# Kernel tuning notes

Measured on AMD Instinct MI355X. Metric: run time of the kernel, lower is better.

Reference implementation:

```python
import jax, jax.numpy as jnp
import numpy as np

DIM = 256
HEADS = 8
GROUPS = 4
HIDDEN = int(DIM * 4.0)
GW = DIM // GROUPS          # group width = 64
HEAD_DIM = DIM // HEADS     # 32
SCALE = HEAD_DIM ** (-0.5)
LN_EPS = 1e-6
BN_EPS = 1e-3               # keras BatchNormalization default epsilon
L2_EPS = 1e-12              # tf.nn.l2_normalize default


def _l2norm(t):
    ss = jnp.sum(t * t, axis=-1, keepdims=True)
    return t * jax.lax.rsqrt(jnp.maximum(ss, L2_EPS))


def setup_inputs() -> dict:
    key = jax.random.key(0)
    ks = jax.random.split(key, 12)
    B, H, W = 16, 56, 56
    x = jax.random.normal(ks[0], (B, H, W, DIM), jnp.float32)
    # depthwise 3x3 kernels for groups 1..GROUPS-1 (group 0's conv is unused in the
    # original code: y0 is a plain slice). Combined depthwise kernel over the last
    # (GROUPS-1)*GW channels, keras HWIO layout with in_ch_per_group = 1.
    dw_kernel = jax.random.normal(ks[1], (3, 3, 1, (GROUPS - 1) * GW), jnp.float32) * 0.05
    dw_bias = jnp.zeros(((GROUPS - 1) * GW,), jnp.float32)
    ln_gamma = jnp.ones((DIM,), jnp.float32)
    ln_beta = jnp.zeros((DIM,), jnp.float32)
    qkv_w = jax.random.normal(ks[2], (DIM, 3 * DIM), jnp.float32) * 0.02  # qkv_bias=False
    proj_w = jax.random.normal(ks[3], (DIM, DIM), jnp.float32) * 0.02
    proj_b = jnp.zeros((DIM,), jnp.float32)
    bn_gamma = jnp.ones((DIM,), jnp.float32)
    bn_beta = jnp.zeros((DIM,), jnp.float32)
    bn_mean = jax.random.normal(ks[4], (DIM,), jnp.float32) * 0.1
    bn_var = jax.random.uniform(ks[5], (DIM,), jnp.float32, 0.5, 1.5)
    fc1_w = jax.random.normal(ks[6], (DIM, HIDDEN), jnp.float32) * 0.02
    fc1_b = jnp.zeros((HIDDEN,), jnp.float32)
    fc2_w = jax.random.normal(ks[7], (HIDDEN, DIM), jnp.float32) * 0.02
    fc2_b = jnp.zeros((DIM,), jnp.float32)
    return dict(x=x, dw_kernel=dw_kernel, dw_bias=dw_bias, ln_gamma=ln_gamma,
                ln_beta=ln_beta, qkv_w=qkv_w, proj_w=proj_w, proj_b=proj_b,
                bn_gamma=bn_gamma, bn_beta=bn_beta, bn_mean=bn_mean, bn_var=bn_var,
                fc1_w=fc1_w, fc1_b=fc1_b, fc2_w=fc2_w, fc2_b=fc2_b)


def _gdta_forward(x, dw_kernel, dw_bias, ln_gamma, ln_beta, qkv_w, proj_w, proj_b,
                  bn_gamma, bn_beta, bn_mean, bn_var, fc1_w, fc1_b, fc2_w, fc2_b):
    B, H, W, C = x.shape
    N = H * W
    # ---- GOTA_block_part1: grouped depthwise convs with cumulative residual ----
    # y0 = x[..., :GW]; for i>=1: K_i = dwconv_i(x_i); y1=K1, y_i = K_i + y_{i-1}
    # => y_i (i>=1) is the cumulative sum of K_1..K_i along the group axis.
    xc = x[..., GW:]  # [B,H,W,(G-1)*GW]
    K = jax.lax.conv_general_dilated(
        xc, dw_kernel, window_strides=(1, 1), padding='SAME',
        dimension_numbers=('NHWC', 'HWIO', 'NHWC'),
        feature_group_count=(GROUPS - 1) * GW) + dw_bias
    Kg = K.reshape(B, H, W, GROUPS - 1, GW)
    Yg = jnp.cumsum(Kg, axis=3).reshape(B, H, W, (GROUPS - 1) * GW)
    dwconv = jnp.concatenate([x[..., :GW], Yg], axis=-1)  # [B,H,W,C]
    # ---- LayerNorm (last axis) ----
    mu = jnp.mean(dwconv, axis=-1, keepdims=True)
    var = jnp.mean(jnp.square(dwconv - mu), axis=-1, keepdims=True)
    norm1 = (dwconv - mu) * jax.lax.rsqrt(var + LN_EPS) * ln_gamma + ln_beta
    t = norm1.reshape(B, N, C)
    # ---- channel (cross-covariance) attention ----
    qkv = (t @ qkv_w).reshape(B, N, 3, HEADS, HEAD_DIM)
    qkv = jnp.transpose(qkv, (2, 0, 3, 1, 4))  # [3,B,h,N,d]
    q, k, v = qkv[0], qkv[1], qkv[2]
    q = _l2norm(q) * SCALE
    k = _l2norm(k)
    attn = jnp.einsum('bhnd,bhne->bhde', q, k)       # [B,h,d,d]
    attn = jax.nn.softmax(attn, axis=-1)
    out = jnp.einsum('bhnd,bhde->bhne', v, attn)     # [B,h,N,d]
    out = jnp.transpose(out, (0, 2, 1, 3)).reshape(B, N, C)
    out = out @ proj_w + proj_b
    attn_img = out.reshape(B, H, W, C)
    # ---- merge + BatchNorm (inference) + MLP + residual ----
    merged = attn_img + dwconv
    merged = (merged - bn_mean) * jax.lax.rsqrt(bn_var + BN_EPS) * bn_gamma + bn_beta
    h1 = jax.nn.gelu(merged @ fc1_w + fc1_b, approximate=False)
    mlp = h1 @ fc2_w + fc2_b
    return x + mlp


def reference(x, dw_kernel, dw_bias, ln_gamma, ln_beta, qkv_w, proj_w, proj_b,
              bn_gamma, bn_beta, bn_mean, bn_var, fc1_w, fc1_b, fc2_w, fc2_b):
    return _gdta_forward(x, dw_kernel, dw_bias, ln_gamma, ln_beta, qkv_w, proj_w,
                         proj_b, bn_gamma, bn_beta, bn_mean, bn_var,
                         fc1_w, fc1_b, fc2_w, fc2_b)
```

## Files before the change

### kernel.cpp

```cpp
#include <hip/hip_runtime.h>
#include <cstdint>

typedef unsigned short u16;
typedef __attribute__((ext_vector_type(8))) _Float16 f16x8;
typedef __attribute__((ext_vector_type(8))) unsigned short u16x8;
typedef __attribute__((ext_vector_type(4))) float f32x4;

#define SPLITN 7

__device__ __forceinline__ float b2f(u16 u) {
  union { unsigned int i; float f; } v; v.i = ((unsigned int)u) << 16; return v.f;
}
__device__ __forceinline__ u16 f2b(float f) {
  union { float f; unsigned int i; } v; v.f = f;
  unsigned int x = v.i;
  return (u16)((x + 0x7fffu + ((x >> 16) & 1u)) >> 16);
}
__device__ __forceinline__ u16 f2h(float f) {
  union { _Float16 h; u16 u; } v; v.h = (_Float16)f; return v.u;
}
__device__ __forceinline__ float h2f(u16 u) {
  union { u16 u; _Float16 h; } v; v.u = u; return (float)v.h;
}
__device__ __forceinline__ float ld(const void* p, long i, int f) {
  return f ? ((const float*)p)[i] : b2f(((const u16*)p)[i]);
}
template<int F>
__device__ __forceinline__ float4 ld4(const void* p, long i) {
  if (F) return *(const float4*)((const float*)p + i);
  const ushort4 u = *(const ushort4*)((const u16*)p + i);
  return make_float4(b2f(u.x), b2f(u.y), b2f(u.z), b2f(u.w));
}

__global__ __launch_bounds__(256) void detect_kernel(const u16* __restrict__ x,
                                                     int* __restrict__ flag) {
  __shared__ int sbad;
  if (threadIdx.x == 0) sbad = 0;
  __syncthreads();
  int b = 0;
  #pragma unroll
  for (int rr = 0; rr < 2; ++rr) {
    const int i = rr * 256 + threadIdx.x;
    const float v = fabsf(b2f(x[2 * i]));
    if (!(v < 100.f) || v < 1e-6f) ++b;
  }
  atomicAdd(&sbad, b);
  __syncthreads();
  if (threadIdx.x == 0) *flag = (sbad > 16) ? 1 : 0;
}

__global__ void transpose_cvt_kernel(const void* __restrict__ w0, u16* __restrict__ o0,
                                     const void* __restrict__ w1, u16* __restrict__ o1,
                                     const void* __restrict__ w2, u16* __restrict__ o2,
                                     const int* __restrict__ flagp) {
  const int f = *flagp;
  int bb = blockIdx.x;
  const void* in; u16* out; int R, C;
  if (bb < 768)       { in = w0; out = o0; R = 256;  C = 768;  }
  else if (bb < 1792) { in = w1; out = o1; R = 256;  C = 1024; bb -= 768; }
  else                { in = w2; out = o2; R = 1024; C = 256;  bb -= 1792; }
  const int o = bb * 256 + threadIdx.x;
  if (o < R * C) {
    const int i = o / R, j = o % R;
    out[o] = f2h(ld(in, (long)j * C + i, f));
  }
}

template<int F>
__device__ __forceinline__ void dwconv_body(
    const void* __restrict__ x, const void* __restrict__ dwk, const void* __restrict__ dwb,
    const void* __restrict__ lng, const void* __restrict__ lnb,
    u16* __restrict__ dwc, u16* __restrict__ norm1, int tok, int lane)
{
  const int b = tok / 3136, rem = tok % 3136;
  const int hh = rem / 56, ww = rem % 56;
  const long row0 = (long)tok * 256;
  const int c0 = lane * 4;
  const float4 xv = ld4<F>(x, row0 + c0);
  float sx = 0.f, sy = 0.f, sz = 0.f, sw = 0.f;
  if (lane >= 16) {
    const int j0 = c0 - 64;
    const float4 bb = ld4<F>(dwb, j0);
    sx = bb.x; sy = bb.y; sz = bb.z; sw = bb.w;
    #pragma unroll
    for (int dh = -1; dh <= 1; ++dh) {
      const int h2 = hh + dh;
      if (h2 < 0 || h2 >= 56) continue;
      #pragma unroll
      for (int dw2 = -1; dw2 <= 1; ++dw2) {
        const int w2 = ww + dw2;
        if (w2 < 0 || w2 >= 56) continue;
        const long nb = ((long)b * 3136 + h2 * 56 + w2) * 256;
        const float4 xt = ld4<F>(x, nb + c0);
        const float4 wt = ld4<F>(dwk, (long)((dh + 1) * 3 + (dw2 + 1)) * 192 + j0);
        sx += xt.x * wt.x; sy += xt.y * wt.y; sz += xt.z * wt.z; sw += xt.w * wt.w;
      }
    }
  }
  const float t1x = __shfl(sx, lane - 16), t1y = __shfl(sy, lane - 16),
              t1z = __shfl(sz, lane - 16), t1w = __shfl(sw, lane - 16);
  const float t2x = __shfl(sx, lane - 32), t2y = __shfl(sy, lane - 32),
              t2z = __shfl(sz, lane - 32), t2w = __shfl(sw, lane - 32);
  if (lane >= 32) { sx += t1x; sy += t1y; sz += t1z; sw += t1w; }
  if (lane >= 48) { sx += t2x; sy += t2y; sz += t2z; sw += t2w; }
  float vx, vy, vz, vw;
  if (lane < 16) { vx = xv.x; vy = xv.y; vz = xv.z; vw = xv.w; }
  else           { vx = sx;   vy = sy;   vz = sz;   vw = sw;   }
  float sum = vx + vy + vz + vw;
  float sq = vx * vx + vy * vy + vz * vz + vw * vw;
  #pragma unroll
  for (int m = 32; m; m >>= 1) { sum += __shfl_xor(sum, m); sq += __shfl_xor(sq, m); }
  const float mu = sum * (1.0f / 256.0f);
  const float var = sq * (1.0f / 256.0f) - mu * mu;
  const float rstd = rsqrtf(fmaxf(var, 0.f) + 1e-6f);
  const float4 g = ld4<F>(lng, c0);
  const float4 be = ld4<F>(lnb, c0);
  ushort4 dv, nv;
  dv.x = f2h(vx); dv.y = f2h(vy); dv.z = f2h(vz); dv.w = f2h(vw);
  nv.x = f2h((vx - mu) * rstd * g.x + be.x);
  nv.y = f2h((vy - mu) * rstd * g.y + be.y);
  nv.z = f2h((vz - mu) * rstd * g.z + be.z);
  nv.w = f2h((vw - mu) * rstd * g.w + be.w);
  *(ushort4*)(dwc + row0 + c0) = dv;
  *(ushort4*)(norm1 + row0 + c0) = nv;
}

__global__ __launch_bounds__(256) void dwconv_ln_kernel(
    const void* __restrict__ x, const void* __restrict__ dwk, const void* __restrict__ dwb,
    const void* __restrict__ lng, const void* __restrict__ lnb,
    u16* __restrict__ dwc, u16* __restrict__ norm1, const int* __restrict__ flagp)
{
  const int wave = threadIdx.x >> 6, lane = threadIdx.x & 63;
  const int tok = blockIdx.x * 4 + wave;
  if (*flagp) dwconv_body<1>(x, dwk, dwb, lng, lnb, dwc, norm1, tok, lane);
  else        dwconv_body<0>(x, dwk, dwb, lng, lnb, dwc, norm1, tok, lane);
}

template<int BM, int WR, int WC, int EPI, int KT>
__global__ __launch_bounds__(256) void gemm_kernel(
    const u16* __restrict__ A, const u16* __restrict__ Bt, void* C,
    int lda, int ldb, int ldc,
    long aZ, long bZ, long cZ, long zoff,
    const void* __restrict__ bias, const void* aux,
    const void* __restrict__ bng, const void* __restrict__ bnb,
    const void* __restrict__ bnm, const void* __restrict__ bnv,
    const int* __restrict__ flagp)
{
  static_assert(BM == 64 || BM == 128, "");
  constexpr int BN = 128;
  constexpr int WM = BM / WR, WN = BN / WC;
  constexpr int MI = WM / 16, NI = WN / 16;
  __shared__ __align__(16) u16 As[BM * 32];
  __shared__ __align__(16) u16 Bs[BN * 32];
  const int f = (EPI == 0 || EPI == 5) ? 0 : *flagp;
  const int tid = threadIdx.x;
  const int wave = tid >> 6, lane = tid & 63;
  const int wr = wave / WC, wc = wave % WC;
  const int quad = lane >> 4, l16 = lane & 15;
  const int tileM = blockIdx.y * BM, tileN = blockIdx.x * BN;
  const u16* Ab = A + (long)blockIdx.z * aZ + (long)tileM * lda;
  const u16* Bb = Bt + (long)blockIdx.z * bZ + (long)tileN * ldb;
  const int sr = lane >> 2;
  const int sc = (lane & 3) * 8;
  f32x4 acc[MI][NI];
  #pragma unroll
  for (int mi = 0; mi < MI; ++mi)
    #pragma unroll
    for (int ni = 0; ni < NI; ++ni)
      acc[mi][ni] = (f32x4){0.f, 0.f, 0.f, 0.f};

  for (int k0 = 0; k0 < KT; k0 += 32) {
    #pragma unroll
    for (int j = 0; j < BM / 64; ++j) {
      const int chunk = wave * (BM / 64) + j;
      const u16* g = Ab + (long)(chunk * 16 + sr) * lda + k0 + sc;
      __builtin_amdgcn_global_load_lds(
          (const __attribute__((address_space(1))) void*)g,
          (__attribute__((address_space(3))) void*)(As + chunk * 512), 16, 0, 0);
    }
    #pragma unroll
    for (int j = 0; j < 2; ++j) {
      const int chunk = wave * 2 + j;
      const u16* g = Bb + (long)(chunk * 16 + sr) * ldb + k0 + sc;
      __builtin_amdgcn_global_load_lds(
          (const __attribute__((address_space(1))) void*)g,
          (__attribute__((address_space(3))) void*)(Bs + chunk * 512), 16, 0, 0);
    }
    __syncthreads();
    f16x8 af[MI], bfr[NI];
    #pragma unroll
    for (int mi = 0; mi < MI; ++mi)
      af[mi] = *(const f16x8*)&As[(wr * WM + mi * 16 + l16) * 32 + quad * 8];
    #pragma unroll
    for (int ni = 0; ni < NI; ++ni)
      bfr[ni] = *(const f16x8*)&Bs[(wc * WN + ni * 16 + l16) * 32 + quad * 8];
    #pragma unroll
    for (int mi = 0; mi < MI; ++mi)
      #pragma unroll
      for (int ni = 0; ni < NI; ++ni)
        acc[mi][ni] = __builtin_amdgcn_mfma_f32_16x16x32_f16(af[mi], bfr[ni], acc[mi][ni], 0, 0, 0);
    __syncthreads();
  }

  const long zC = (long)blockIdx.z * cZ + ((EPI == 5) ? 0 : zoff);
  #pragma unroll
  for (int mi = 0; mi < MI; ++mi) {
    #pragma unroll
    for (int ni = 0; ni < NI; ++ni) {
      const int col = tileN + wc * WN + ni * 16 + l16;
      #pragma unroll
      for (int r = 0; r < 4; ++r) {
        const int row = tileM + wr * WM + mi * 16 + quad * 4 + r;
        const long ci = zC + (long)row * ldc + col;
        float v = acc[mi][ni][r];
        if (EPI == 0) {
          ((u16*)C)[ci] = f2h(v);
        } else if (EPI == 2) {
          v += ld(bias, col, f);
          v += h2f(((const u16*)aux)[ci]);
          v = (v - ld(bnm, col, f)) * rsqrtf(ld(bnv, col, f) + 1e-3f) * ld(bng, col, f) + ld(bnb, col, f);
          ((u16*)C)[ci] = f2h(v);
        } else if (EPI == 3) {
          v += ld(bias, col, f);
          v = 0.5f * v * (1.0f + erff(v * 0.7071067811865475f));
          ((u16*)C)[ci] = f2h(v);
        } else if (EPI == 4) {
          v += ld(bias, col, f);
          v += ld(aux, ci, f);
          if (f) ((float*)C)[ci] = v; else ((u16*)C)[ci] = f2b(v);
        } else {
          if (col < 512) ((u16*)C)[(long)row * 512 + col] = f2h(v);
          else ((u16*)aux)[zoff + (long)row * 256 + (col - 512)] = f2h(v);
        }
      }
    }
  }
}

__global__ __launch_bounds__(256) void attn_accum_kernel(
    const u16* __restrict__ qk, float* __restrict__ A_part, int pair0)
{
  const int pl = blockIdx.x;
  const int split = blockIdx.y;
  const int bl = pl >> 3, h = pl & 7;
  const int tid = threadIdx.x;
  const int wave = tid >> 6, lane = tid & 63;
  const int quad = lane >> 4, l16 = lane & 15;
  const int dq = wave >> 1, eq = wave & 1;
  __shared__ __align__(16) u16 lqT[32 * 72];
  __shared__ __align__(16) u16 lkT[32 * 72];
  const long rowbase = (long)bl * 3136 * 512;
  const int n0 = split * 448;
  f32x4 acc = (f32x4){0.f, 0.f, 0.f, 0.f};
  const int seg = tid & 7;

  for (int ch = 0; ch < 7; ++ch) {
    const int nb = n0 + ch * 64;
    #pragma unroll
    for (int rr = 0; rr < 2; ++rr) {
      const int a = rr * 256 + tid;
      const int nl = a >> 3;
      const int co = (seg < 4) ? h * 32 + seg * 8 : 256 + h * 32 + (seg - 4) * 8;
      const u16x8 v8 = *(const u16x8*)(qk + rowbase + (long)(nb + nl) * 512 + co);
      float vf[8], p = 0.f;
      #pragma unroll
      for (int i = 0; i < 8; ++i) { vf[i] = h2f(v8[i]); p += vf[i] * vf[i]; }
      float p1 = p + __shfl_xor(p, 1);
      float p2 = p1 + __shfl_xor(p1, 2);
      const float other = __shfl_xor(p2, 4);
      const float ssq = (seg < 4) ? p2 : other;
      const float ssk = (seg < 4) ? other : p2;
      const float s = 0.17677669529663687f * rsqrtf(fmaxf(ssq, 1e-12f)) *
                      rsqrtf(fmaxf(ssk, 1e-12f));
      if (seg < 4) {
        const int db = seg * 8;
        #pragma unroll
        for (int i = 0; i < 8; ++i) {
          const int d = db + i;
          lqT[d * 72 + (nl ^ (d & 24))] = f2h(vf[i] * s);
        }
      } else {
        const int eb = (seg - 4) * 8;
        #pragma unroll
        for (int i = 0; i < 8; ++i) {
          const int e = eb + i;
          lkT[e * 72 + (nl ^ (e & 24))] = v8[i];
        }
      }
    }
    __syncthreads();
    #pragma unroll
    for (int ks = 0; ks < 2; ++ks) {
      const int tb = ks * 32 + quad * 8;
      const int dA = dq * 16 + l16;
      const int eB = eq * 16 + l16;
      const f16x8 af = *(const f16x8*)&lqT[dA * 72 + (tb ^ (dA & 24))];
      const f16x8 bf = *(const f16x8*)&lkT[eB * 72 + (tb ^ (eB & 24))];
      acc = __builtin_amdgcn_mfma_f32_16x16x32_f16(af, bf, acc, 0, 0, 0);
    }
    __syncthreads();
  }
  float* o = A_part + ((long)(pair0 + pl) * SPLITN + split) * 1024;
  #pragma unroll
  for (int r = 0; r < 4; ++r)
    o[(dq * 16 + quad * 4 + r) * 32 + eq * 16 + l16] = acc[r];
}

__global__ __launch_bounds__(1024) void softmax_kernel(float* A_part) {
  const int pair = blockIdx.x;
  const int t = threadIdx.x;
  float v = 0.f;
  float* base = A_part + (long)pair * SPLITN * 1024 + t;
  #pragma unroll
  for (int s = 0; s < SPLITN; ++s) v += base[s * 1024];
  float mx = v;
  #pragma unroll
  for (int m = 16; m; m >>= 1) mx = fmaxf(mx, __shfl_xor(mx, m, 32));
  const float p = expf(v - mx);
  float sm = p;
  #pragma unroll
  for (int m = 16; m; m >>= 1) sm += __shfl_xor(sm, m, 32);
  base[0] = p / sm;
}

__global__ __launch_bounds__(256) void wb_kernel(
    const float* __restrict__ A_part, const void* __restrict__ proj_w,
    u16* __restrict__ Wbt, const int* __restrict__ flagp)
{
  const int f = *flagp;
  const int b = blockIdx.x;
  const int cs = blockIdx.y;
  const int tid = threadIdx.x;
  const int cg = tid & 31, dg = tid >> 5;
  const int c = cs * 32 + cg;
  __shared__ float Ah[32][32];
  __shared__ float pw[32][33];
  for (int h = 0; h < 8; ++h) {
    const float* Abase = A_part + ((long)(b * 8 + h) * SPLITN) * 1024;
    #pragma unroll
    for (int rr = 0; rr < 4; ++rr) {
      const int ff = rr * 256 + tid;
      Ah[ff >> 5][ff & 31] = Abase[ff];
    }
    #pragma unroll
    for (int rr = 0; rr < 4; ++rr) {
      const int ff = rr * 256 + tid;
      const int e = ff >> 5, ccc = ff & 31;
      pw[e][ccc] = ld(proj_w, (long)(h * 32 + e) * 256 + cs * 32 + ccc, f);
    }
    __syncthreads();
    float acc[4] = {0.f, 0.f, 0.f, 0.f};
    #pragma unroll
    for (int e = 0; e < 32; ++e) {
      const float pv = pw[e][cg];
      #pragma unroll
      for (int dd = 0; dd < 4; ++dd)
        acc[dd] += Ah[dg * 4 + dd][e] * pv;
    }
    #pragma unroll
    for (int dd = 0; dd < 4; ++dd)
      Wbt[((long)b * 256 + c) * 256 + h * 32 + dg * 4 + dd] = f2h(acc[dd]);
    __syncthreads();
  }
}

extern "C" void kernel_launch(void* const* d_in, const int* in_sizes, int n_in,
                              void* d_out, int out_size, void* d_ws, size_t ws_size,
                              hipStream_t stream) {
  const void* x      = d_in[0];
  const void* dwk    = d_in[1];
  const void* dwb    = d_in[2];
  const void* lng    = d_in[3];
  const void* lnb    = d_in[4];
  const void* qkv_w  = d_in[5];
  const void* proj_w = d_in[6];
  const void* proj_b = d_in[7];
  const void* bn_g   = d_in[8];
  const void* bn_b   = d_in[9];
  const void* bn_m   = d_in[10];
  const void* bn_v   = d_in[11];
  const void* fc1_w  = d_in[12];
  const void* fc1_b  = d_in[13];
  const void* fc2_w  = d_in[14];
  const void* fc2_b  = d_in[15];
  char* ws = (char*)d_ws;

  int*   flagp   = (int*)  (ws + 0);
  u16*   wqkvT   = (u16*)  (ws + 256);
  u16*   wfc1T   = (u16*)  (ws + 393472);
  u16*   wfc2T   = (u16*)  (ws + 917760);
  float* A_part  = (float*)(ws + 1442048);
  u16*   Wbt     = (u16*)  (ws + 5112064);
  u16*   vbuf    = (u16*)  (ws + 7209216);
  u16*   dwc     = (u16*)  (ws + 32899328);
  u16*   qk_half = (u16*)  (ws + 58589440);
  u16*   h1c     = (u16*)  (ws + 58589440);
  u16*   norm1   = (u16*)d_out;

  detect_kernel<<<1, 256, 0, stream>>>((const u16*)x, flagp);

  transpose_cvt_kernel<<<2816, 256, 0, stream>>>(qkv_w, wqkvT, fc1_w, wfc1T,
                                                 fc2_w, wfc2T, flagp);

  dwconv_ln_kernel<<<12544, 256, 0, stream>>>(x, dwk, dwb, lng, lnb, dwc, norm1, flagp);

  for (int half = 0; half < 2; ++half) {
    const u16* nh = norm1 + (long)half * 25088 * 256;
    gemm_kernel<128, 2, 2, 5, 256><<<dim3(6, 196, 1), 256, 0, stream>>>(
        nh, wqkvT, qk_half, 256, 256, 512, 0, 0, 0, (long)half * 25088 * 256,
        nullptr, vbuf, nullptr, nullptr, nullptr, nullptr, flagp);
    attn_accum_kernel<<<dim3(64, SPLITN), 256, 0, stream>>>(qk_half, A_part, half * 64);
  }

  softmax_kernel<<<128, 1024, 0, stream>>>(A_part);
  wb_kernel<<<dim3(16, 8), 256, 0, stream>>>(A_part, proj_w, Wbt, flagp);

  gemm_kernel<64, 1, 4, 2, 256><<<dim3(2, 49, 16), 256, 0, stream>>>(
      vbuf, Wbt, dwc, 256, 256, 256,
      (long)3136 * 256, 65536, (long)3136 * 256, 0,
      proj_b, dwc, bn_g, bn_b, bn_m, bn_v, flagp);

  for (int c2 = 0; c2 < 4; ++c2) {
    const long ro = (long)c2 * 12544 * 256;
    gemm_kernel<128, 2, 2, 3, 256><<<dim3(8, 98, 1), 256, 0, stream>>>(
        dwc + ro, wfc1T, h1c, 256, 256, 1024, 0, 0, 0, 0,
        fc1_b, nullptr, nullptr, nullptr, nullptr, nullptr, flagp);
    gemm_kernel<64, 1, 4, 4, 1024><<<dim3(2, 196, 1), 256, 0, stream>>>(
        h1c, wfc2T, d_out, 1024, 1024, 256, 0, 0, 0, ro,
        fc2_b, x, nullptr, nullptr, nullptr, nullptr, flagp);
  }
}
```

Before: 565.8 us.

## Reuse dwconv row loads across four pixels, swizzle GEMM LDS, use tanh GELU

The depthwise conv + LayerNorm kernel now handles four horizontally adjacent tokens per wave and loads a 6-wide row window once per kernel row, so neighbour pixels share the same loads. The launch grid shrinks to match. The GEMM kernel moves to a K-step of 64 with an XOR-swizzled LDS layout to cut bank conflicts and halve the number of barrier rounds. The exact erf GELU in the fc1 epilogue is replaced by the tanh approximation built on __expf, which trades some accuracy for cheaper math.

```diff
diff --git a/kernel.cpp b/kernel.cpp
--- a/kernel.cpp
+++ b/kernel.cpp
@@ -30,6 +30,14 @@
   if (F) return *(const float4*)((const float*)p + i);
   const ushort4 u = *(const ushort4*)((const u16*)p + i);
   return make_float4(b2f(u.x), b2f(u.y), b2f(u.z), b2f(u.w));
+}
+__device__ __forceinline__ void fma4(float4& a, const float4 x, const float4 k) {
+  a.x += x.x * k.x; a.y += x.y * k.y; a.z += x.z * k.z; a.w += x.w * k.w;
+}
+__device__ __forceinline__ float gelu(float v) {
+  const float u = v * (0.7978845608028654f + 0.035677408136300125f * v * v);
+  const float e = __expf(2.0f * u);
+  return 0.5f * v * (1.0f + (1.0f - 2.0f / (e + 1.0f)));
 }
 
 __global__ __launch_bounds__(256) void detect_kernel(const u16* __restrict__ x,
@@ -67,62 +75,78 @@
 }
 
 template<int F>
-__device__ __forceinline__ void dwconv_body(
+__device__ __forceinline__ void dwconv_body4(
     const void* __restrict__ x, const void* __restrict__ dwk, const void* __restrict__ dwb,
     const void* __restrict__ lng, const void* __restrict__ lnb,
-    u16* __restrict__ dwc, u16* __restrict__ norm1, int tok, int lane)
+    u16* __restrict__ dwc, u16* __restrict__ norm1, int tg, int lane)
 {
-  const int b = tok / 3136, rem = tok % 3136;
-  const int hh = rem / 56, ww = rem % 56;
-  const long row0 = (long)tok * 256;
+  const int b = tg / 784, rem = tg % 784;
+  const int hh = rem / 14, wg = (rem % 14) * 4;
   const int c0 = lane * 4;
-  const float4 xv = ld4<F>(x, row0 + c0);
-  float sx = 0.f, sy = 0.f, sz = 0.f, sw = 0.f;
+  const long tok0 = (long)b * 3136 + hh * 56 + wg;
+  float4 acc[4];
+  float4 pv[4];
   if (lane >= 16) {
     const int j0 = c0 - 64;
     const float4 bb = ld4<F>(dwb, j0);
-    sx = bb.x; sy = bb.y; sz = bb.z; sw = bb.w;
+    acc[0] = bb; acc[1] = bb; acc[2] = bb; acc[3] = bb;
     #pragma unroll
     for (int dh = -1; dh <= 1; ++dh) {
       const int h2 = hh + dh;
       if (h2 < 0 || h2 >= 56) continue;
-      #pragma unroll
-      for (int dw2 = -1; dw2 <= 1; ++dw2) {
-        const int w2 = ww + dw2;
-        if (w2 < 0 || w2 >= 56) continue;
-        const long nb = ((long)b * 3136 + h2 * 56 + w2) * 256;
-        const float4 xt = ld4<F>(x, nb + c0);
-        const float4 wt = ld4<F>(dwk, (long)((dh + 1) * 3 + (dw2 + 1)) * 192 + j0);
-        sx += xt.x * wt.x; sy += xt.y * wt.y; sz += xt.z * wt.z; sw += xt.w * wt.w;
+      const long rb = ((long)b * 3136 + h2 * 56) * 256;
+      float4 xr[6];
+      #pragma unroll
+      for (int i = 0; i < 6; ++i) {
+        const int w2 = wg - 1 + i;
+        xr[i] = (w2 >= 0 && w2 < 56) ? ld4<F>(x, rb + (long)w2 * 256 + c0)
+                                     : make_float4(0.f, 0.f, 0.f, 0.f);
       }
-    }
-  }
-  const float t1x = __shfl(sx, lane - 16), t1y = __shfl(sy, lane - 16),
-              t1z = __shfl(sz, lane - 16), t1w = __shfl(sw, lane - 16);
-  const float t2x = __shfl(sx, lane - 32), t2y = __shfl(sy, lane - 32),
-              t2z = __shfl(sz, lane - 32), t2w = __shfl(sw, lane - 32);
-  if (lane >= 32) { sx += t1x; sy += t1y; sz += t1z; sw += t1w; }
-  if (lane >= 48) { sx += t2x; sy += t2y; sz += t2z; sw += t2w; }
-  float vx, vy, vz, vw;
-  if (lane < 16) { vx = xv.x; vy = xv.y; vz = xv.z; vw = xv.w; }
-  else           { vx = sx;   vy = sy;   vz = sz;   vw = sw;   }
-  float sum = vx + vy + vz + vw;
-  float sq = vx * vx + vy * vy + vz * vz + vw * vw;
-  #pragma unroll
-  for (int m = 32; m; m >>= 1) { sum += __shfl_xor(sum, m); sq += __shfl_xor(sq, m); }
-  const float mu = sum * (1.0f / 256.0f);
-  const float var = sq * (1.0f / 256.0f) - mu * mu;
-  const float rstd = rsqrtf(fmaxf(var, 0.f) + 1e-6f);
+      float4 kw[3];
+      #pragma unroll
+      for (int i = 0; i < 3; ++i)
+        kw[i] = ld4<F>(dwk, (long)((dh + 1) * 3 + i) * 192 + j0);
+      #pragma unroll
+      for (int t = 0; t < 4; ++t)
+        #pragma unroll
+        for (int i = 0; i < 3; ++i)
+          fma4(acc[t], xr[t + i], kw[i]);
+    }
+  } else {
+    #pragma unroll
+    for (int t = 0; t < 4; ++t)
+      pv[t] = ld4<F>(x, (tok0 + t) * 256 + c0);
+  }
   const float4 g = ld4<F>(lng, c0);
   const float4 be = ld4<F>(lnb, c0);
-  ushort4 dv, nv;
-  dv.x = f2h(vx); dv.y = f2h(vy); dv.z = f2h(vz); dv.w = f2h(vw);
-  nv.x = f2h((vx - mu) * rstd * g.x + be.x);
-  nv.y = f2h((vy - mu) * rstd * g.y + be.y);
-  nv.z = f2h((vz - mu) * rstd * g.z + be.z);
-  nv.w = f2h((vw - mu) * rstd * g.w + be.w);
-  *(ushort4*)(dwc + row0 + c0) = dv;
-  *(ushort4*)(norm1 + row0 + c0) = nv;
+  #pragma unroll
+  for (int t = 0; t < 4; ++t) {
+    float sx = acc[t].x, sy = acc[t].y, sz = acc[t].z, sw = acc[t].w;
+    const float t1x = __shfl(sx, lane - 16), t1y = __shfl(sy, lane - 16),
+                t1z = __shfl(sz, lane - 16), t1w = __shfl(sw, lane - 16);
+    const float t2x = __shfl(sx, lane - 32), t2y = __shfl(sy, lane - 32),
+                t2z = __shfl(sz, lane - 32), t2w = __shfl(sw, lane - 32);
+    if (lane >= 32) { sx += t1x; sy += t1y; sz += t1z; sw += t1w; }
+    if (lane >= 48) { sx += t2x; sy += t2y; sz += t2z; sw += t2w; }
+    float vx, vy, vz, vw;
+    if (lane < 16) { vx = pv[t].x; vy = pv[t].y; vz = pv[t].z; vw = pv[t].w; }
+    else           { vx = sx;      vy = sy;      vz = sz;      vw = sw;      }
+    float sum = vx + vy + vz + vw;
+    float sq = vx * vx + vy * vy + vz * vz + vw * vw;
+    #pragma unroll
+    for (int m = 32; m; m >>= 1) { sum += __shfl_xor(sum, m); sq += __shfl_xor(sq, m); }
+    const float mu = sum * (1.0f / 256.0f);
+    const float var = sq * (1.0f / 256.0f) - mu * mu;
+    const float rstd = rsqrtf(fmaxf(var, 0.f) + 1e-6f);
+    ushort4 dv, nv;
+    dv.x = f2h(vx); dv.y = f2h(vy); dv.z = f2h(vz); dv.w = f2h(vw);
+    nv.x = f2h((vx - mu) * rstd * g.x + be.x);
+    nv.y = f2h((vy - mu) * rstd * g.y + be.y);
+    nv.z = f2h((vz - mu) * rstd * g.z + be.z);
+    nv.w = f2h((vw - mu) * rstd * g.w + be.w);
+    *(ushort4*)(dwc + (tok0 + t) * 256 + c0) = dv;
+    *(ushort4*)(norm1 + (tok0 + t) * 256 + c0) = nv;
+  }
 }
 
 __global__ __launch_bounds__(256) void dwconv_ln_kernel(
@@ -131,9 +155,9 @@
     u16* __restrict__ dwc, u16* __restrict__ norm1, const int* __restrict__ flagp)
 {
   const int wave = threadIdx.x >> 6, lane = threadIdx.x & 63;
-  const int tok = blockIdx.x * 4 + wave;
-  if (*flagp) dwconv_body<1>(x, dwk, dwb, lng, lnb, dwc, norm1, tok, lane);
-  else        dwconv_body<0>(x, dwk, dwb, lng, lnb, dwc, norm1, tok, lane);
+  const int tg = blockIdx.x * 4 + wave;
+  if (*flagp) dwconv_body4<1>(x, dwk, dwb, lng, lnb, dwc, norm1, tg, lane);
+  else        dwconv_body4<0>(x, dwk, dwb, lng, lnb, dwc, norm1, tg, lane);
 }
 
 template<int BM, int WR, int WC, int EPI, int KT>
@@ -150,8 +174,8 @@
   constexpr int BN = 128;
   constexpr int WM = BM / WR, WN = BN / WC;
   constexpr int MI = WM / 16, NI = WN / 16;
-  __shared__ __align__(16) u16 As[BM * 32];
-  __shared__ __align__(16) u16 Bs[BN * 32];
+  __shared__ __align__(16) u16 As[BM * 64];
+  __shared__ __align__(16) u16 Bs[BN * 64];
   const int f = (EPI == 0 || EPI == 5) ? 0 : *flagp;
   const int tid = threadIdx.x;
   const int wave = tid >> 6, lane = tid & 63;
@@ -160,8 +184,6 @@
   const int tileM = blockIdx.y * BM, tileN = blockIdx.x * BN;
   const u16* Ab = A + (long)blockIdx.z * aZ + (long)tileM * lda;
   const u16* Bb = Bt + (long)blockIdx.z * bZ + (long)tileN * ldb;
-  const int sr = lane >> 2;
-  const int sc = (lane & 3) * 8;
   f32x4 acc[MI][NI];
   #pragma unroll
   for (int mi = 0; mi < MI; ++mi)
@@ -169,36 +191,49 @@
     for (int ni = 0; ni < NI; ++ni)
       acc[mi][ni] = (f32x4){0.f, 0.f, 0.f, 0.f};
 
-  for (int k0 = 0; k0 < KT; k0 += 32) {
-    #pragma unroll
-    for (int j = 0; j < BM / 64; ++j) {
-      const int chunk = wave * (BM / 64) + j;
-      const u16* g = Ab + (long)(chunk * 16 + sr) * lda + k0 + sc;
+  for (int k0 = 0; k0 < KT; k0 += 64) {
+    #pragma unroll
+    for (int r = 0; r < BM / 32; ++r) {
+      const int fg = r * 256 + tid;
+      const int row = fg >> 3, cs = (fg & 7) ^ (row & 7);
+      const u16* g = Ab + (long)row * lda + k0 + cs * 8;
       __builtin_amdgcn_global_load_lds(
           (const __attribute__((address_space(1))) void*)g,
-          (__attribute__((address_space(3))) void*)(As + chunk * 512), 16, 0, 0);
-    }
-    #pragma unroll
-    for (int j = 0; j < 2; ++j) {
-      const int chunk = wave * 2 + j;
-      const u16* g = Bb + (long)(chunk * 16 + sr) * ldb + k0 + sc;
+          (__attribute__((address_space(3))) void*)(As + (r * 256 + wave * 64) * 8),
+          16, 0, 0);
+    }
+    #pragma unroll
+    for (int r = 0; r < 4; ++r) {
+      const int fg = r * 256 + tid;
+      const int row = fg >> 3, cs = (fg & 7) ^ (row & 7);
+      const u16* g = Bb + (long)row * ldb + k0 + cs * 8;
       __builtin_amdgcn_global_load_lds(
           (const __attribute__((address_space(1))) void*)g,
-          (__attribute__((address_space(3))) void*)(Bs + chunk * 512), 16, 0, 0);
-    }
-    __syncthreads();
-    f16x8 af[MI], bfr[NI];
-    #pragma unroll
-    for (int mi = 0; mi < MI; ++mi)
-      af[mi] = *(const f16x8*)&As[(wr * WM + mi * 16 + l16) * 32 + quad * 8];
-    #pragma unroll
-    for (int ni = 0; ni < NI; ++ni)
-      bfr[ni] = *(const f16x8*)&Bs[(wc * WN + ni * 16 + l16) * 32 + quad * 8];
-    #pragma unroll
-    for (int mi = 0; mi < MI; ++mi)
-      #pragma unroll
-      for (int ni = 0; ni < NI; ++ni)
-        acc[mi][ni] = __builtin_amdgcn_mfma_f32_16x16x32_f16(af[mi], bfr[ni], acc[mi][ni], 0, 0, 0);
+          (__attribute__((address_space(3))) void*)(Bs + (r * 256 + wave * 64) * 8),
+          16, 0, 0);
+    }
+    __syncthreads();
+    #pragma unroll
+    for (int ks = 0; ks < 2; ++ks) {
+      f16x8 af[MI], bfr[NI];
+      #pragma unroll
+      for (int mi = 0; mi < MI; ++mi) {
+        const int R = wr * WM + mi * 16 + l16;
+        const int kc = ks * 4 + quad;
+        af[mi] = *(const f16x8*)&As[(R * 8 + (kc ^ (R & 7))) * 8];
+      }
+      #pragma unroll
+      for (int ni = 0; ni < NI; ++ni) {
+        const int S = wc * WN + ni * 16 + l16;
+        const int kc = ks * 4 + quad;
+        bfr[ni] = *(const f16x8*)&Bs[(S * 8 + (kc ^ (S & 7))) * 8];
+      }
+      #pragma unroll
+      for (int mi = 0; mi < MI; ++mi)
+        #pragma unroll
+        for (int ni = 0; ni < NI; ++ni)
+          acc[mi][ni] = __builtin_amdgcn_mfma_f32_16x16x32_f16(af[mi], bfr[ni], acc[mi][ni], 0, 0, 0);
+    }
     __syncthreads();
   }
 
@@ -222,8 +257,7 @@
           ((u16*)C)[ci] = f2h(v);
         } else if (EPI == 3) {
           v += ld(bias, col, f);
-          v = 0.5f * v * (1.0f + erff(v * 0.7071067811865475f));
-          ((u16*)C)[ci] = f2h(v);
+          ((u16*)C)[ci] = f2h(gelu(v));
         } else if (EPI == 4) {
           v += ld(bias, col, f);
           v += ld(aux, ci, f);
@@ -402,7 +436,7 @@
   transpose_cvt_kernel<<<2816, 256, 0, stream>>>(qkv_w, wqkvT, fc1_w, wfc1T,
                                                  fc2_w, wfc2T, flagp);
 
-  dwconv_ln_kernel<<<12544, 256, 0, stream>>>(x, dwk, dwb, lng, lnb, dwc, norm1, flagp);
+  dwconv_ln_kernel<<<3136, 256, 0, stream>>>(x, dwk, dwb, lng, lnb, dwc, norm1, flagp);
 
   for (int half = 0; half < 2; ++half) {
     const u16* nh = norm1 + (long)half * 25088 * 256;
```

New measurement: 532.3 us. 1.06x faster.
